# Optimization experiments

Measured on AMD Instinct MI355X. Metric: run time of the kernel, lower is better.

## Reference

```python
import jax, jax.numpy as jnp
import numpy as np

N = 50000
E = 800000
IN_F = 128
HID_F = 128
OUT_F = 64


def setup_inputs() -> dict:
    key = jax.random.key(0)
    ks = jax.random.split(key, 12)
    x = jax.random.normal(ks[0], (N, IN_F), dtype=jnp.float32)
    row0 = jax.random.randint(ks[1], (E,), 0, N, dtype=jnp.int32)
    col0 = jax.random.randint(ks[2], (E,), 0, N, dtype=jnp.int32)
    val0 = jax.random.uniform(ks[3], (E,), dtype=jnp.float32)
    row1 = jax.random.randint(ks[4], (E,), 0, N, dtype=jnp.int32)
    col1 = jax.random.randint(ks[5], (E,), 0, N, dtype=jnp.int32)
    val1 = jax.random.uniform(ks[6], (E,), dtype=jnp.float32)
    # GraphConvolution params, uniform(-stdv, stdv) with stdv = 1/sqrt(out_features)
    s0 = 1.0 / np.sqrt(HID_F)
    W0 = jax.random.uniform(ks[7], (IN_F, HID_F), minval=-s0, maxval=s0, dtype=jnp.float32)
    b0 = jax.random.uniform(ks[8], (HID_F,), minval=-s0, maxval=s0, dtype=jnp.float32)
    s1 = 1.0 / np.sqrt(OUT_F)
    W1 = jax.random.uniform(ks[9], (HID_F, OUT_F), minval=-s1, maxval=s1, dtype=jnp.float32)
    b1 = jax.random.uniform(ks[10], (OUT_F,), minval=-s1, maxval=s1, dtype=jnp.float32)
    return {"x": x, "row0": row0, "col0": col0, "val0": val0,
            "row1": row1, "col1": col1, "val1": val1,
            "W0": W0, "b0": b0, "W1": W1, "b1": b1}


def _gcn_layer(x, W, b, row, col, val):
    # support = x @ W ; out = spmm(adj, support) + b
    support = x @ W                       # [N, F_out]
    msgs = val[:, None] * support[col]    # [E, F_out] gather along edges
    out = jax.ops.segment_sum(msgs, row, num_segments=N)
    return out + b


def reference(x, row0, col0, val0, row1, col1, val1, W0, b0, W1, b1):
    # Layer 0: GC -> relu (dropout is identity in eval mode)
    h = _gcn_layer(x, W0, b0, row0, col0, val0)
    h = jax.nn.relu(h)
    # Layer 1 (final): GC only
    out = _gcn_layer(h, W1, b1, row1, col1, val1)
    return out
```

## Files before the change

kernel.cpp:

```cpp
#include <hip/hip_runtime.h>
#include <hip/hip_fp16.h>
#include <type_traits>

#define N_NODES 50000
#define IN_F    128
#define HID_F   128
#define OUT_F   64
#define E_EDGES 800000

#define RPB   128
#define NBUCK ((N_NODES + RPB - 1) / RPB)
#define BCAP  2560
#define BIN_T   512
#define BIN_EPT 16
#define BIN_EPB (BIN_T * BIN_EPT)
#define BIN_NB  ((E_EDGES + BIN_EPB - 1) / BIN_EPB)

typedef _Float16 half8 __attribute__((ext_vector_type(8)));
typedef float    floatx4 __attribute__((ext_vector_type(4)));

__global__ __launch_bounds__(256) void prep_kernel(const float* __restrict__ W0,
                                                   const float* __restrict__ W1,
                                                   __half* __restrict__ wt0,
                                                   __half* __restrict__ wt1,
                                                   int* __restrict__ gfill) {
    int tid = blockIdx.x * 256 + threadIdx.x;
    if (tid < IN_F * HID_F) {
        int k = tid >> 7, n = tid & 127;
        wt0[n * IN_F + k] = __float2half(W0[tid]);
    }
    if (tid < HID_F * OUT_F) {
        int k = tid / OUT_F, n = tid % OUT_F;
        wt1[n * HID_F + k] = __float2half(W1[tid]);
    }
    if (tid < 2 * NBUCK) gfill[tid] = 0;
}

template<int K, int NF, bool RELU_A, typename AT>
__global__ __launch_bounds__(256) void gemm_mfma_kernel(const AT* __restrict__ A,
                                                        const __half* __restrict__ Wt,
                                                        __half* __restrict__ C, int M) {
    constexpr int KP = K + 8;
    constexpr int NT = NF / 16;
    __shared__ _Float16 Ws[NF * KP];
    const int tid = threadIdx.x;
    constexpr int CH = NF * K / 8;
    for (int c = tid; c < CH; c += 256) {
        const int n = c / (K / 8), ko = (c % (K / 8)) * 8;
        *(half8*)&Ws[n * KP + ko] = *(const half8*)(Wt + n * K + ko);
    }
    __syncthreads();

    const int wv = tid >> 6, lane = tid & 63;
    const int quad = lane >> 4, l16 = lane & 15;
    const int rowb = blockIdx.x * 64 + wv * 16;
    const int arow = rowb + l16;

    floatx4 acc[NT] = {};
#pragma unroll
    for (int ks = 0; ks < K; ks += 32) {
        half8 af = {};
        if (arow < M) {
            if constexpr (std::is_same<AT, float>::value) {
                const float4* p = (const float4*)(A + (long)arow * K + ks + quad * 8);
                float4 u = p[0], w = p[1];
                af[0] = (_Float16)u.x; af[1] = (_Float16)u.y;
                af[2] = (_Float16)u.z; af[3] = (_Float16)u.w;
                af[4] = (_Float16)w.x; af[5] = (_Float16)w.y;
                af[6] = (_Float16)w.z; af[7] = (_Float16)w.w;
            } else {
                af = *(const half8*)(A + (long)arow * K + ks + quad * 8);
            }
        }
        if (RELU_A) {
            _Float16 z = (_Float16)0;
#pragma unroll
            for (int j = 0; j < 8; ++j) af[j] = af[j] > z ? af[j] : z;
        }
#pragma unroll
        for (int t = 0; t < NT; ++t) {
            half8 bf = *(const half8*)&Ws[(t * 16 + l16) * KP + ks + quad * 8];
            acc[t] = __builtin_amdgcn_mfma_f32_16x16x32_f16(af, bf, acc[t], 0, 0, 0);
        }
    }
#pragma unroll
    for (int t = 0; t < NT; ++t) {
        const int col = t * 16 + l16;
#pragma unroll
        for (int i = 0; i < 4; ++i) {
            const int row = rowb + quad * 4 + i;
            if (row < M) C[(long)row * NF + col] = __float2half(acc[t][i]);
        }
    }
}

__global__ __launch_bounds__(BIN_T) void bin_kernel(
        const int* __restrict__ row0, const int* __restrict__ col0, const float* __restrict__ val0,
        const int* __restrict__ row1, const int* __restrict__ col1, const float* __restrict__ val1,
        int* __restrict__ gfill, int2* __restrict__ bcv0, int2* __restrict__ bcv1) {
    const int g = blockIdx.y;
    const int*   rowi = g ? row1 : row0;
    const int*   coli = g ? col1 : col0;
    const float* vali = g ? val1 : val0;
    int*  gf  = gfill + g * NBUCK;
    int2* bcv = g ? bcv1 : bcv0;

    __shared__ int lhist[NBUCK];
    __shared__ int lbase[NBUCK];
    const int tid = threadIdx.x;
    for (int i = tid; i < NBUCK; i += BIN_T) lhist[i] = 0;
    __syncthreads();

    int rnk[BIN_EPT], bkt[BIN_EPT], cl[BIN_EPT], rw[BIN_EPT];
    float vl[BIN_EPT];
    const int e0 = blockIdx.x * BIN_EPB;
#pragma unroll
    for (int i = 0; i < BIN_EPT; ++i) {
        const int e = e0 + i * BIN_T + tid;
        bkt[i] = -1;
        if (e < E_EDGES) {
            const int r = rowi[e];
            rw[i] = r; cl[i] = coli[e]; vl[i] = vali[e];
            const int b = r / RPB;
            bkt[i] = b;
            rnk[i] = atomicAdd(&lhist[b], 1);
        }
    }
    __syncthreads();
    for (int i = tid; i < NBUCK; i += BIN_T) {
        const int c = lhist[i];
        lbase[i] = c ? atomicAdd(&gf[i], c) : 0;
    }
    __syncthreads();
#pragma unroll
    for (int i = 0; i < BIN_EPT; ++i) {
        if (bkt[i] >= 0) {
            const int pos = lbase[bkt[i]] + rnk[i];
            if (pos < BCAP)
                bcv[(long)bkt[i] * BCAP + pos] =
                    make_int2(((rw[i] & (RPB - 1)) << 16) | cl[i], __float_as_int(vl[i]));
        }
    }
}

#define MID_T 512
#define SORT_EPT (BCAP / MID_T)
union MidLds {
    struct {
        int2 sbuf[BCAP];
        int  cur[RPB];
        int  sc[RPB];
        int  start[RPB + 1];
    } s;
    _Float16 ws[HID_F * (IN_F + 8)];
};

__global__ __launch_bounds__(MID_T) void mid_kernel(
        const int* __restrict__ gfill, int2* __restrict__ bcv0, int2* __restrict__ bcv1,
        int* __restrict__ rs0, int* __restrict__ rs1,
        const float* __restrict__ x, const __half* __restrict__ wt0,
        __half* __restrict__ sup0, int M) {
    __shared__ MidLds lds;
    const int tid = threadIdx.x;

    if (blockIdx.y < 2) {
        const int g = blockIdx.y;
        const int b = blockIdx.x;
        int2* buf = (g ? bcv1 : bcv0) + (long)b * BCAP;
        int*  rs  = (g ? rs1 : rs0) + b * (RPB + 1);

        int cnt = gfill[g * NBUCK + b];
        if (cnt > BCAP) cnt = BCAP;

        int2 ed[SORT_EPT];
#pragma unroll
        for (int k = 0; k < SORT_EPT; ++k) {
            const int e = tid + k * MID_T;
            if (e < cnt) ed[k] = buf[e];
        }

        if (tid < RPB) lds.s.cur[tid] = 0;
        __syncthreads();
#pragma unroll
        for (int k = 0; k < SORT_EPT; ++k)
            if (tid + k * MID_T < cnt) atomicAdd(&lds.s.cur[ed[k].x >> 16], 1);
        __syncthreads();
        if (tid < RPB) lds.s.sc[tid] = lds.s.cur[tid];
        __syncthreads();
        for (int off = 1; off < RPB; off <<= 1) {
            int v = 0;
            if (tid < RPB && tid >= off) v = lds.s.sc[tid - off];
            __syncthreads();
            if (tid < RPB) lds.s.sc[tid] += v;
            __syncthreads();
        }
        if (tid < RPB) {
            lds.s.start[tid + 1] = lds.s.sc[tid];
            if (tid == 0) lds.s.start[0] = 0;
            lds.s.cur[tid] = (tid == 0) ? 0 : lds.s.sc[tid - 1];
        }
        __syncthreads();
#pragma unroll
        for (int k = 0; k < SORT_EPT; ++k) {
            if (tid + k * MID_T < cnt) {
                int pos = atomicAdd(&lds.s.cur[ed[k].x >> 16], 1);
                lds.s.sbuf[pos] = ed[k];
            }
        }
        __syncthreads();
#pragma unroll
        for (int k = 0; k < SORT_EPT; ++k) {
            const int e = tid + k * MID_T;
            if (e < cnt) buf[e] = lds.s.sbuf[e];
        }
        for (int i = tid; i <= RPB; i += MID_T) rs[i] = lds.s.start[i];
    } else {
        constexpr int KP = IN_F + 8;
        constexpr int NT = HID_F / 16;
        for (int c = tid; c < HID_F * (IN_F / 8); c += MID_T) {
            const int n = c / (IN_F / 8), ko = (c % (IN_F / 8)) * 8;
            *(half8*)&lds.ws[n * KP + ko] = *(const half8*)(wt0 + n * IN_F + ko);
        }
        __syncthreads();

        const int wv = tid >> 6, lane = tid & 63;
        const int quad = lane >> 4, l16 = lane & 15;
        const int rowb = blockIdx.x * 128 + wv * 16;
        const int arow = rowb + l16;

        floatx4 acc[NT] = {};
#pragma unroll
        for (int ks = 0; ks < IN_F; ks += 32) {
            half8 af = {};
            if (arow < M) {
                const float4* p = (const float4*)(x + (long)arow * IN_F + ks + quad * 8);
                float4 u = p[0], w = p[1];
                af[0] = (_Float16)u.x; af[1] = (_Float16)u.y;
                af[2] = (_Float16)u.z; af[3] = (_Float16)u.w;
                af[4] = (_Float16)w.x; af[5] = (_Float16)w.y;
                af[6] = (_Float16)w.z; af[7] = (_Float16)w.w;
            }
#pragma unroll
            for (int t = 0; t < NT; ++t) {
                half8 bf = *(const half8*)&lds.ws[(t * 16 + l16) * KP + ks + quad * 8];
                acc[t] = __builtin_amdgcn_mfma_f32_16x16x32_f16(af, bf, acc[t], 0, 0, 0);
            }
        }
#pragma unroll
        for (int t = 0; t < NT; ++t) {
            const int col = t * 16 + l16;
#pragma unroll
            for (int i = 0; i < 4; ++i) {
                const int row = rowb + quad * 4 + i;
                if (row < M) sup0[(long)row * HID_F + col] = __float2half(acc[t][i]);
            }
        }
    }
}

__global__ __launch_bounds__(256) void spmm_l0_kernel(const int* __restrict__ rs,
                                                      const int2* __restrict__ bcv,
                                                      const __half* __restrict__ sup,
                                                      const float* __restrict__ bias,
                                                      __half* __restrict__ out, int n) {
    const int wave = threadIdx.x >> 6;
    const int lane = threadIdx.x & 63;
    const int r = blockIdx.x * 4 + wave;
    if (r >= n) return;
    const int b  = r >> 7;
    const int rl = r & (RPB - 1);
    const int* rsb = rs + b * (RPB + 1);
    const int start = rsb[rl];
    const int end   = rsb[rl + 1];
    const int2* eb = bcv + (long)b * BCAP;
    const int f0 = lane * 2;
    float acc0 = bias[f0];
    float acc1 = bias[f0 + 1];

    for (int base = start; base < end; base += 64) {
        const int m = min(64, end - base);
        int2 cvl = make_int2(0, 0);
        if (lane < m) cvl = eb[base + lane];
        for (int j = 0; j < m; j += 8) {
            int   p[8];
            float v[8];
#pragma unroll
            for (int q = 0; q < 8; ++q) {
                p[q] = __shfl(cvl.x, j + q, 64);
                v[q] = __int_as_float(__shfl(cvl.y, j + q, 64));
            }
            __half2 s[8];
#pragma unroll
            for (int q = 0; q < 8; ++q)
                s[q] = *(const __half2*)(sup + (long)(p[q] & 0xFFFF) * HID_F + f0);
#pragma unroll
            for (int q = 0; q < 8; ++q) {
                float2 gq = __half22float2(s[q]);
                acc0 += v[q] * gq.x; acc1 += v[q] * gq.y;
            }
        }
    }
    *(__half2*)(out + (long)r * HID_F + f0) = __floats2half2_rn(acc0, acc1);
}

__global__ __launch_bounds__(256) void spmm_l1_kernel(const int* __restrict__ rs,
                                                      const int2* __restrict__ bcv,
                                                      const __half* __restrict__ sup,
                                                      const float* __restrict__ bias,
                                                      float* __restrict__ out, int n) {
    const int wave = threadIdx.x >> 6;
    const int lane = threadIdx.x & 63;
    const int r = blockIdx.x * 4 + wave;
    if (r >= n) return;
    const int b  = r >> 7;
    const int rl = r & (RPB - 1);
    const int* rsb = rs + b * (RPB + 1);
    const int start = rsb[rl];
    const int end   = rsb[rl + 1];
    const int2* eb = bcv + (long)b * BCAP;
    const int eh = lane >> 5;
    const int li = lane & 31;
    const int f0 = li * 2;
    float acc0 = eh ? 0.f : bias[f0];
    float acc1 = eh ? 0.f : bias[f0 + 1];

    for (int base = start; base < end; base += 64) {
        const int m = min(64, end - base);
        int2 cvl = make_int2(0, 0);
        if (lane < m) cvl = eb[base + lane];
        for (int j = 0; j < m; j += 16) {
            int   p[8];
            float v[8];
#pragma unroll
            for (int q = 0; q < 8; ++q) {
                const int src = j + 2 * q + eh;
                p[q] = __shfl(cvl.x, src, 64);
                v[q] = __int_as_float(__shfl(cvl.y, src, 64));
            }
            __half2 s[8];
#pragma unroll
            for (int q = 0; q < 8; ++q)
                s[q] = *(const __half2*)(sup + (long)(p[q] & 0xFFFF) * OUT_F + f0);
#pragma unroll
            for (int q = 0; q < 8; ++q) {
                float2 gq = __half22float2(s[q]);
                acc0 += v[q] * gq.x; acc1 += v[q] * gq.y;
            }
        }
    }
    acc0 += __shfl_xor(acc0, 32, 64);
    acc1 += __shfl_xor(acc1, 32, 64);
    if (eh == 0)
        *(float2*)(out + (long)r * OUT_F + f0) = make_float2(acc0, acc1);
}

extern "C" void kernel_launch(void* const* d_in, const int* in_sizes, int n_in,
                              void* d_out, int out_size, void* d_ws, size_t ws_size,
                              hipStream_t stream) {
    const float* x    = (const float*)d_in[0];
    const int*   row0 = (const int*)d_in[1];
    const int*   col0 = (const int*)d_in[2];
    const float* val0 = (const float*)d_in[3];
    const int*   row1 = (const int*)d_in[4];
    const int*   col1 = (const int*)d_in[5];
    const float* val1 = (const float*)d_in[6];
    const float* W0   = (const float*)d_in[7];
    const float* b0   = (const float*)d_in[8];
    const float* W1   = (const float*)d_in[9];
    const float* b1   = (const float*)d_in[10];
    float* out = (float*)d_out;

    const int M = N_NODES;

    __half* sup0 = (__half*)d_ws;
    __half* h    = sup0 + (long)N_NODES * HID_F;
    int2* bcv0   = (int2*)(h + (long)N_NODES * HID_F);
    int2* bcv1   = bcv0 + (long)NBUCK * BCAP;
    int*  rs0    = (int*)(bcv1 + (long)NBUCK * BCAP);
    int*  rs1    = rs0 + NBUCK * (RPB + 1);
    int*  gfill  = rs1 + NBUCK * (RPB + 1);
    __half* wt0  = (__half*)(gfill + 2 * NBUCK + 2);
    __half* wt1  = wt0 + IN_F * HID_F;
    __half* sup1 = sup0;

    const int SPMM_B = (N_NODES + 3) / 4;

    prep_kernel<<<(IN_F * HID_F + 255) / 256, 256, 0, stream>>>(W0, W1, wt0, wt1, gfill);
    bin_kernel<<<dim3(BIN_NB, 2), BIN_T, 0, stream>>>(row0, col0, val0, row1, col1, val1,
                                                      gfill, bcv0, bcv1);
    mid_kernel<<<dim3(NBUCK, 3), MID_T, 0, stream>>>(gfill, bcv0, bcv1, rs0, rs1,
                                                     x, wt0, sup0, M);

    spmm_l0_kernel<<<SPMM_B, 256, 0, stream>>>(rs0, bcv0, sup0, b0, h, N_NODES);

    gemm_mfma_kernel<HID_F, OUT_F, true, __half><<<(M + 63) / 64, 256, 0, stream>>>(h, wt1, sup1, M);
    spmm_l1_kernel<<<SPMM_B, 256, 0, stream>>>(rs1, bcv1, sup1, b1, out, N_NODES);
}
```

Measured before the change: 182.5 us.

## Fuse layer-0 SpMM, ReLU and layer-1 GEMM into one kernel

Replaces the separate layer-0 aggregation kernel and the layer-1 MFMA GEMM with one kernel. Each block aggregates 16 rows (4 per wave), applies bias and ReLU, stages the hidden rows in LDS, then runs a 16x64 MFMA against W1 read directly from global memory. This drops the round trip of the hidden activation through HBM and one kernel launch. In exchange each wave now handles 4 rows serially, blocks are smaller in output work, and sup1 gets its own buffer instead of aliasing sup0.

```diff
diff --git a/kernel.cpp b/kernel.cpp
--- a/kernel.cpp
+++ b/kernel.cpp
@@ -1,6 +1,5 @@
 #include <hip/hip_runtime.h>
 #include <hip/hip_fp16.h>
-#include <type_traits>
 
 #define N_NODES 50000
 #define IN_F    128
@@ -34,64 +33,6 @@
         wt1[n * HID_F + k] = __float2half(W1[tid]);
     }
     if (tid < 2 * NBUCK) gfill[tid] = 0;
-}
-
-template<int K, int NF, bool RELU_A, typename AT>
-__global__ __launch_bounds__(256) void gemm_mfma_kernel(const AT* __restrict__ A,
-                                                        const __half* __restrict__ Wt,
-                                                        __half* __restrict__ C, int M) {
-    constexpr int KP = K + 8;
-    constexpr int NT = NF / 16;
-    __shared__ _Float16 Ws[NF * KP];
-    const int tid = threadIdx.x;
-    constexpr int CH = NF * K / 8;
-    for (int c = tid; c < CH; c += 256) {
-        const int n = c / (K / 8), ko = (c % (K / 8)) * 8;
-        *(half8*)&Ws[n * KP + ko] = *(const half8*)(Wt + n * K + ko);
-    }
-    __syncthreads();
-
-    const int wv = tid >> 6, lane = tid & 63;
-    const int quad = lane >> 4, l16 = lane & 15;
-    const int rowb = blockIdx.x * 64 + wv * 16;
-    const int arow = rowb + l16;
-
-    floatx4 acc[NT] = {};
-#pragma unroll
-    for (int ks = 0; ks < K; ks += 32) {
-        half8 af = {};
-        if (arow < M) {
-            if constexpr (std::is_same<AT, float>::value) {
-                const float4* p = (const float4*)(A + (long)arow * K + ks + quad * 8);
-                float4 u = p[0], w = p[1];
-                af[0] = (_Float16)u.x; af[1] = (_Float16)u.y;
-                af[2] = (_Float16)u.z; af[3] = (_Float16)u.w;
-                af[4] = (_Float16)w.x; af[5] = (_Float16)w.y;
-                af[6] = (_Float16)w.z; af[7] = (_Float16)w.w;
-            } else {
-                af = *(const half8*)(A + (long)arow * K + ks + quad * 8);
-            }
-        }
-        if (RELU_A) {
-            _Float16 z = (_Float16)0;
-#pragma unroll
-            for (int j = 0; j < 8; ++j) af[j] = af[j] > z ? af[j] : z;
-        }
-#pragma unroll
-        for (int t = 0; t < NT; ++t) {
-            half8 bf = *(const half8*)&Ws[(t * 16 + l16) * KP + ks + quad * 8];
-            acc[t] = __builtin_amdgcn_mfma_f32_16x16x32_f16(af, bf, acc[t], 0, 0, 0);
-        }
-    }
-#pragma unroll
-    for (int t = 0; t < NT; ++t) {
-        const int col = t * 16 + l16;
-#pragma unroll
-        for (int i = 0; i < 4; ++i) {
-            const int row = rowb + quad * 4 + i;
-            if (row < M) C[(long)row * NF + col] = __float2half(acc[t][i]);
-        }
-    }
 }
 
 __global__ __launch_bounds__(BIN_T) void bin_kernel(
@@ -258,49 +199,73 @@
     }
 }
 
-__global__ __launch_bounds__(256) void spmm_l0_kernel(const int* __restrict__ rs,
-                                                      const int2* __restrict__ bcv,
-                                                      const __half* __restrict__ sup,
-                                                      const float* __restrict__ bias,
-                                                      __half* __restrict__ out, int n) {
-    const int wave = threadIdx.x >> 6;
+__global__ __launch_bounds__(256) void agg_gemm_kernel(const int* __restrict__ rs,
+                                                       const int2* __restrict__ bcv,
+                                                       const __half* __restrict__ sup,
+                                                       const float* __restrict__ bias,
+                                                       const __half* __restrict__ wt1,
+                                                       __half* __restrict__ sup1) {
+    constexpr int HP = HID_F + 8;
+    __shared__ _Float16 ht[16 * HP];
+    const int wv   = threadIdx.x >> 6;
     const int lane = threadIdx.x & 63;
-    const int r = blockIdx.x * 4 + wave;
-    if (r >= n) return;
-    const int b  = r >> 7;
-    const int rl = r & (RPB - 1);
+    const int r0 = blockIdx.x * 16;
+    const int b  = r0 >> 7;
     const int* rsb = rs + b * (RPB + 1);
-    const int start = rsb[rl];
-    const int end   = rsb[rl + 1];
     const int2* eb = bcv + (long)b * BCAP;
     const int f0 = lane * 2;
-    float acc0 = bias[f0];
-    float acc1 = bias[f0 + 1];
-
-    for (int base = start; base < end; base += 64) {
-        const int m = min(64, end - base);
-        int2 cvl = make_int2(0, 0);
-        if (lane < m) cvl = eb[base + lane];
-        for (int j = 0; j < m; j += 8) {
-            int   p[8];
-            float v[8];
-#pragma unroll
-            for (int q = 0; q < 8; ++q) {
-                p[q] = __shfl(cvl.x, j + q, 64);
-                v[q] = __int_as_float(__shfl(cvl.y, j + q, 64));
-            }
-            __half2 s[8];
-#pragma unroll
-            for (int q = 0; q < 8; ++q)
-                s[q] = *(const __half2*)(sup + (long)(p[q] & 0xFFFF) * HID_F + f0);
-#pragma unroll
-            for (int q = 0; q < 8; ++q) {
-                float2 gq = __half22float2(s[q]);
-                acc0 += v[q] * gq.x; acc1 += v[q] * gq.y;
-            }
-        }
-    }
-    *(__half2*)(out + (long)r * HID_F + f0) = __floats2half2_rn(acc0, acc1);
+
+#pragma unroll
+    for (int i = 0; i < 4; ++i) {
+        const int rl = (r0 & (RPB - 1)) + wv * 4 + i;
+        const int start = rsb[rl];
+        const int end   = rsb[rl + 1];
+        float acc0 = bias[f0];
+        float acc1 = bias[f0 + 1];
+        for (int base = start; base < end; base += 64) {
+            const int m = min(64, end - base);
+            int2 cvl = make_int2(0, 0);
+            if (lane < m) cvl = eb[base + lane];
+            for (int j = 0; j < m; j += 8) {
+                int   p[8];
+                float v[8];
+#pragma unroll
+                for (int q = 0; q < 8; ++q) {
+                    p[q] = __shfl(cvl.x, j + q, 64);
+                    v[q] = __int_as_float(__shfl(cvl.y, j + q, 64));
+                }
+                __half2 s[8];
+#pragma unroll
+                for (int q = 0; q < 8; ++q)
+                    s[q] = *(const __half2*)(sup + (long)(p[q] & 0xFFFF) * HID_F + f0);
+#pragma unroll
+                for (int q = 0; q < 8; ++q) {
+                    float2 gq = __half22float2(s[q]);
+                    acc0 += v[q] * gq.x; acc1 += v[q] * gq.y;
+                }
+            }
+        }
+        acc0 = acc0 > 0.f ? acc0 : 0.f;
+        acc1 = acc1 > 0.f ? acc1 : 0.f;
+        _Float16 h2[2] = { (_Float16)acc0, (_Float16)acc1 };
+        *(_Float16*)&ht[(wv * 4 + i) * HP + f0]     = h2[0];
+        *(_Float16*)&ht[(wv * 4 + i) * HP + f0 + 1] = h2[1];
+    }
+    __syncthreads();
+
+    const int quad = lane >> 4, l16 = lane & 15;
+    floatx4 acc = {};
+#pragma unroll
+    for (int ks = 0; ks < HID_F; ks += 32) {
+        half8 af = *(const half8*)&ht[l16 * HP + ks + quad * 8];
+        half8 bf = *(const half8*)(wt1 + (long)(wv * 16 + l16) * HID_F + ks + quad * 8);
+        acc = __builtin_amdgcn_mfma_f32_16x16x32_f16(af, bf, acc, 0, 0, 0);
+    }
+#pragma unroll
+    for (int i = 0; i < 4; ++i) {
+        const int row = r0 + quad * 4 + i;
+        sup1[(long)row * OUT_F + wv * 16 + l16] = __float2half(acc[i]);
+    }
 }
 
 __global__ __launch_bounds__(256) void spmm_l1_kernel(const int* __restrict__ rs,
@@ -373,15 +338,14 @@
     const int M = N_NODES;
 
     __half* sup0 = (__half*)d_ws;
-    __half* h    = sup0 + (long)N_NODES * HID_F;
-    int2* bcv0   = (int2*)(h + (long)N_NODES * HID_F);
+    __half* sup1 = sup0 + (long)N_NODES * HID_F;
+    int2* bcv0   = (int2*)(sup1 + (long)N_NODES * HID_F);
     int2* bcv1   = bcv0 + (long)NBUCK * BCAP;
     int*  rs0    = (int*)(bcv1 + (long)NBUCK * BCAP);
     int*  rs1    = rs0 + NBUCK * (RPB + 1);
     int*  gfill  = rs1 + NBUCK * (RPB + 1);
     __half* wt0  = (__half*)(gfill + 2 * NBUCK + 2);
     __half* wt1  = wt0 + IN_F * HID_F;
-    __half* sup1 = sup0;
 
     const int SPMM_B = (N_NODES + 3) / 4;
 
@@ -391,8 +355,7 @@
     mid_kernel<<<dim3(NBUCK, 3), MID_T, 0, stream>>>(gfill, bcv0, bcv1, rs0, rs1,
                                                      x, wt0, sup0, M);
 
-    spmm_l0_kernel<<<SPMM_B, 256, 0, stream>>>(rs0, bcv0, sup0, b0, h, N_NODES);
-
-    gemm_mfma_kernel<HID_F, OUT_F, true, __half><<<(M + 63) / 64, 256, 0, stream>>>(h, wt1, sup1, M);
+    agg_gemm_kernel<<<N_NODES / 16, 256, 0, stream>>>(rs0, bcv0, sup0, b0, wt1, sup1);
+
     spmm_l1_kernel<<<SPMM_B, 256, 0, stream>>>(rs1, bcv1, sup1, b1, out, N_NODES);
 }
```

After: 179.8 us. No clear change (-1.5%).
